# Performance work log

Hardware: AMD Instinct MI355X
Metric: run time of the kernel (lower is better)

Reference implementation:

```python
import jax, jax.numpy as jnp
import numpy as np

N = 100000          # nodes
E = 1600000         # edges (avg degree 16)
IN_DIM = 64
HID = 64
OUT = 32
NUM_GRAPHS = 64


def setup_inputs() -> dict:
    key = jax.random.key(0)
    ks = jax.random.split(key, 12)
    x = jax.random.normal(ks[0], (N, IN_DIM), dtype=jnp.float32)
    edge_index = jax.random.randint(ks[1], (2, E), 0, N, dtype=jnp.int64)
    batch = jnp.sort(jax.random.randint(ks[2], (N,), 0, NUM_GRAPHS, dtype=jnp.int64))
    s = 0.05
    return {
        "x": x,
        "edge_index": edge_index,
        "batch": batch,
        "w1_init": jax.random.normal(ks[3], (IN_DIM, HID), dtype=jnp.float32) * s,
        "w1_root": jax.random.normal(ks[4], (IN_DIM, HID), dtype=jnp.float32) * s,
        "b1": jnp.zeros((HID,), dtype=jnp.float32),
        "w2_init": jax.random.normal(ks[5], (HID, HID), dtype=jnp.float32) * s,
        "w2_root": jax.random.normal(ks[6], (HID, HID), dtype=jnp.float32) * s,
        "b2": jnp.zeros((HID,), dtype=jnp.float32),
        "fc_w": jax.random.normal(ks[7], (HID, OUT), dtype=jnp.float32) * s,
        "fc_b": jnp.zeros((OUT,), dtype=jnp.float32),
    }


def reference(x, edge_index, batch, w1_init, w1_root, b1, w2_init, w2_root, b2, fc_w, fc_b):
    row, col = edge_index[0], edge_index[1]
    # gcn_norm without self loops (ARMAConv default): deg over target nodes
    ones_e = jnp.ones((E,), dtype=x.dtype)
    deg = jax.ops.segment_sum(ones_e, col, num_segments=N)
    dinv = jnp.where(deg > 0, jax.lax.rsqrt(jnp.maximum(deg, 1.0)), 0.0)
    norm = dinv[row] * dinv[col]  # [E]

    def propagate(h):  # out[col] += norm * h[row]
        return jax.ops.segment_sum(h[row] * norm[:, None], col, num_segments=N)

    # ARMAConv (K=1, T=1, act=None): A_hat (x W_init) + x W_root + b
    h = jax.nn.relu(propagate(x @ w1_init) + x @ w1_root + b1)
    h = jax.nn.relu(propagate(h @ w2_init) + h @ w2_root + b2)

    # global mean pool over graphs
    cnt = jax.ops.segment_sum(jnp.ones((N,), dtype=h.dtype), batch, num_segments=NUM_GRAPHS)
    pooled = jax.ops.segment_sum(h, batch, num_segments=NUM_GRAPHS) / jnp.maximum(cnt, 1.0)[:, None]

    return pooled @ fc_w + fc_b  # [NUM_GRAPHS, OUT]
```

## Files before the change

kernel.cpp:

```cpp
#include <hip/hip_runtime.h>
#include <hip/hip_bf16.h>


#define NB 256
#define CAP 5120
#define MAXB 400
#define P1_CHUNK 2048

typedef unsigned int uint32;
typedef unsigned short ushort16;
typedef __attribute__((ext_vector_type(8))) short short8;
typedef __attribute__((ext_vector_type(4))) float f32x4;

__device__ inline uint32 bf16rn(float f) {
    uint32 u = __float_as_uint(f);
    uint32 r = ((u >> 16) & 1u) + 0x7FFFu;
    return (u + r) >> 16;
}
__device__ inline uint32 pack_bf16(float a, float b) {
    return bf16rn(a) | (bf16rn(b) << 16);
}
__device__ inline float bflo(uint32 u) { return __uint_as_float(u << 16); }
__device__ inline float bfhi(uint32 u) { return __uint_as_float(u & 0xFFFF0000u); }

__global__ __launch_bounds__(256) void bucket_kernel(
    const int* __restrict__ row, const int* __restrict__ col,
    uint32* __restrict__ bpack, int* __restrict__ bcnt, int E,
    const float* __restrict__ W1i, const float* __restrict__ W1r,
    const float* __restrict__ W2i, const float* __restrict__ W2r,
    ushort16* __restrict__ wt) {
    __shared__ int hist[MAXB];
    __shared__ int ofs[MAXB];
    __shared__ int cur[MAXB];
    __shared__ int gbase[MAXB];
    __shared__ int s[256];
    __shared__ uint32 stage[P1_CHUNK];
    __shared__ unsigned short stage_bk[P1_CHUNK];

    int t = threadIdx.x;

    if (blockIdx.x < 128) {
        int idx = blockIdx.x * 256 + t;
        int m = idx >> 12;
        int r = idx & 4095;
        int d = r >> 6, k = r & 63;
        const float* W = (m < 2) ? W1i : (m < 4) ? W1r : (m < 6) ? W2i : W2r;
        float v = W[k * 64 + d];
        uint32 hi = bf16rn(v);
        uint32 outv;
        if (m & 1) {
            float hf = __uint_as_float(hi << 16);
            outv = bf16rn(v - hf);
        } else {
            outv = hi;
        }
        wt[(size_t)m * 4096 + d * 64 + k] = (unsigned short)outv;
        return;
    }

    for (int i = t; i < MAXB; i += 256) hist[i] = 0;
    __syncthreads();

    int e0 = (blockIdx.x - 128) * P1_CHUNK;
    int cntE = min(E - e0, P1_CHUNK);

    for (int i = t; i < cntE; i += 256) {
        int c = col[e0 + i];
        atomicAdd(&hist[c >> 8], 1);
    }
    __syncthreads();

    int i2 = 2 * t;
    int a = (i2 < MAXB) ? hist[i2] : 0;
    int b = (i2 + 1 < MAXB) ? hist[i2 + 1] : 0;
    s[t] = a + b;
    __syncthreads();
    for (int off = 1; off < 256; off <<= 1) {
        int x = (t >= off) ? s[t - off] : 0;
        __syncthreads();
        s[t] += x;
        __syncthreads();
    }
    int excl = (t > 0) ? s[t - 1] : 0;
    if (i2 < MAXB) ofs[i2] = excl;
    if (i2 + 1 < MAXB) ofs[i2 + 1] = excl + a;
    __syncthreads();

    for (int i = t; i < MAXB; i += 256) {
        cur[i] = ofs[i];
        gbase[i] = hist[i] ? atomicAdd(&bcnt[i], hist[i]) : 0;
    }
    __syncthreads();

    for (int i = t; i < cntE; i += 256) {
        int c = col[e0 + i];
        int r = row[e0 + i];
        int bk = c >> 8;
        int k = atomicAdd(&cur[bk], 1);
        stage[k] = ((uint32)(c & 255) << 24) | (uint32)r;
        stage_bk[k] = (unsigned short)bk;
    }
    __syncthreads();

    for (int i = t; i < cntE; i += 256) {
        uint32 pk = stage[i];
        int bk = stage_bk[i];
        int gd = gbase[bk] + (i - ofs[bk]);
        if (gd < CAP) bpack[(size_t)bk * CAP + gd] = pk;
    }
}

__global__ __launch_bounds__(1024) void csr_gemm(
    const uint32* __restrict__ bpack, const int* __restrict__ bcnt,
    int* __restrict__ es, int* __restrict__ nstart, int* __restrict__ ndeg,
    float* __restrict__ dinv,
    const float* __restrict__ X, const ushort16* __restrict__ wt4,
    const float* __restrict__ bias,
    ushort16* __restrict__ Ts, ushort16* __restrict__ Rs, int n) {
    __shared__ int h[NB];
    __shared__ alignas(16) unsigned char uni[36864];
    uint32* sbp = (uint32*)uni;
    int* s      = (int*)(uni + 20480);
    int* cur    = (int*)(uni + 21504);
    unsigned short* sXs = (unsigned short*)uni;

    int b = blockIdx.x, t = threadIdx.x;
    if (t < NB) h[t] = 0;
    __syncthreads();
    int cnt = min(bcnt[b], CAP);
    size_t base = (size_t)b * CAP;
    for (int i = t; i < cnt; i += 1024) {
        uint32 pk = bpack[base + i];
        sbp[i] = pk;
        atomicAdd(&h[pk >> 24], 1);
    }
    __syncthreads();
    if (t < NB) s[t] = h[t];
    __syncthreads();
    for (int off = 1; off < NB; off <<= 1) {
        int x = 0;
        if (t < NB && t >= off) x = s[t - off];
        __syncthreads();
        if (t < NB) s[t] += x;
        __syncthreads();
    }
    if (t < NB) {
        int myofs = s[t] - h[t];
        cur[t] = myofs;
        int node = b * NB + t;
        if (node < n) {
            nstart[node] = (int)base + myofs;
            ndeg[node] = h[t];
            dinv[node] = h[t] ? rsqrtf((float)h[t]) : 0.0f;
        }
    }
    __syncthreads();
    for (int i = t; i < cnt; i += 1024) {
        uint32 pk = sbp[i];
        int cl = (int)(pk >> 24);
        int p = atomicAdd(&cur[cl], 1);
        es[base + p] = (int)(pk & 0xFFFFFFu);
    }
    __syncthreads();

    for (int i = t; i < 4096; i += 1024) {
        int tile = i >> 10, j = i & 1023;
        int r = j >> 4, c4 = (j & 15) * 4;
        int node = b * NB + tile * 64 + r;
        float4 v = make_float4(0.f, 0.f, 0.f, 0.f);
        if (node < n) v = *(const float4*)&X[(size_t)node * 64 + c4];
        *(uint32*)&sXs[tile * 4608 + r * 72 + c4] = pack_bf16(v.x, v.y);
        *(uint32*)&sXs[tile * 4608 + r * 72 + c4 + 2] = pack_bf16(v.z, v.w);
    }
    __syncthreads();

    int wv = t >> 6, lane = t & 63;
    int tile = wv >> 2, wq = wv & 3;
    int q = lane >> 4, colx = lane & 15;
    int dim = wq * 16 + colx;

    short8 bih[2], bil[2], brh[2], brl[2];
#pragma unroll
    for (int kh = 0; kh < 2; ++kh) {
        size_t o = (size_t)dim * 64 + kh * 32 + q * 8;
        bih[kh] = *(const short8*)&wt4[0 * 4096 + o];
        bil[kh] = *(const short8*)&wt4[1 * 4096 + o];
        brh[kh] = *(const short8*)&wt4[2 * 4096 + o];
        brl[kh] = *(const short8*)&wt4[3 * 4096 + o];
    }
    float4 bias4 = *(const float4*)&bias[wq * 16 + q * 4];

    unsigned short* TsU = (unsigned short*)Ts;
    unsigned short* RsU = (unsigned short*)Rs;

#pragma unroll
    for (int mt = 0; mt < 4; ++mt) {
        int rbase = mt * 16 + colx;
        short8 a0 = *(const short8*)&sXs[tile * 4608 + rbase * 72 + q * 8];
        short8 a1 = *(const short8*)&sXs[tile * 4608 + rbase * 72 + 32 + q * 8];
        f32x4 accT = {0.f, 0.f, 0.f, 0.f};
        f32x4 accR = {0.f, 0.f, 0.f, 0.f};
        accT = __builtin_amdgcn_mfma_f32_16x16x32_bf16(bih[0], a0, accT, 0, 0, 0);
        accT = __builtin_amdgcn_mfma_f32_16x16x32_bf16(bih[1], a1, accT, 0, 0, 0);
        accT = __builtin_amdgcn_mfma_f32_16x16x32_bf16(bil[0], a0, accT, 0, 0, 0);
        accT = __builtin_amdgcn_mfma_f32_16x16x32_bf16(bil[1], a1, accT, 0, 0, 0);
        accR = __builtin_amdgcn_mfma_f32_16x16x32_bf16(brh[0], a0, accR, 0, 0, 0);
        accR = __builtin_amdgcn_mfma_f32_16x16x32_bf16(brh[1], a1, accR, 0, 0, 0);
        accR = __builtin_amdgcn_mfma_f32_16x16x32_bf16(brl[0], a0, accR, 0, 0, 0);
        accR = __builtin_amdgcn_mfma_f32_16x16x32_bf16(brl[1], a1, accR, 0, 0, 0);

        int li = tile * 64 + mt * 16 + colx;
        int node = b * NB + li;
        if (node < n) {
            int dg = h[li];
            float dv = dg ? rsqrtf((float)dg) : 0.0f;
            uint2 pT, pR;
            pT.x = pack_bf16(accT[0] * dv, accT[1] * dv);
            pT.y = pack_bf16(accT[2] * dv, accT[3] * dv);
            pR.x = pack_bf16(accR[0] + bias4.x, accR[1] + bias4.y);
            pR.y = pack_bf16(accR[2] + bias4.z, accR[3] + bias4.w);
            size_t o = (size_t)node * 64 + wq * 16 + q * 4;
            *(uint2*)&TsU[o] = pT;
            *(uint2*)&RsU[o] = pR;
        }
    }
}

__global__ __launch_bounds__(256) void gather_gemm(
    const uint2* __restrict__ Ts2, const uint2* __restrict__ Rs2,
    const int* __restrict__ es, const int* __restrict__ nstart,
    const int* __restrict__ ndeg, const float* __restrict__ dinv,
    const ushort16* __restrict__ wt4, const float* __restrict__ bias,
    ushort16* __restrict__ To, ushort16* __restrict__ Ro, int n) {
    __shared__ unsigned short sHs[64 * 72];
    int t = threadIdx.x;
    int w = t >> 6, lane = t & 63;
    int q = lane >> 4, d4 = lane & 15;
    int node0 = blockIdx.x * 64;

    for (int rd = 0; rd < 16; ++rd) {
        int cl = w * 16 + rd;
        int c = node0 + cl;
        if (c < n) {
            int deg = ndeg[c];
            int s0 = nstart[c];
            float a0 = 0.f, a1 = 0.f, a2 = 0.f, a3 = 0.f;
            for (int base = 0; base < deg; base += 64) {
                int m = min(deg - base, 64);
                int sid = (lane < m) ? es[s0 + base + lane] : 0;
                for (int j = 0; j < m; j += 16) {
                    int e0 = j + q, e1 = j + 4 + q, e2 = j + 8 + q, e3 = j + 12 + q;
                    int r0 = __shfl(sid, e0);
                    int r1 = __shfl(sid, e1);
                    int r2 = __shfl(sid, e2);
                    int r3 = __shfl(sid, e3);
                    uint2 z = make_uint2(0u, 0u);
                    uint2 v0 = (e0 < m) ? Ts2[(size_t)r0 * 16 + d4] : z;
                    uint2 v1 = (e1 < m) ? Ts2[(size_t)r1 * 16 + d4] : z;
                    uint2 v2 = (e2 < m) ? Ts2[(size_t)r2 * 16 + d4] : z;
                    uint2 v3 = (e3 < m) ? Ts2[(size_t)r3 * 16 + d4] : z;
                    a0 += bflo(v0.x) + bflo(v1.x) + bflo(v2.x) + bflo(v3.x);
                    a1 += bfhi(v0.x) + bfhi(v1.x) + bfhi(v2.x) + bfhi(v3.x);
                    a2 += bflo(v0.y) + bflo(v1.y) + bflo(v2.y) + bflo(v3.y);
                    a3 += bfhi(v0.y) + bfhi(v1.y) + bfhi(v2.y) + bfhi(v3.y);
                }
            }
            a0 += __shfl_xor(a0, 16); a0 += __shfl_xor(a0, 32);
            a1 += __shfl_xor(a1, 16); a1 += __shfl_xor(a1, 32);
            a2 += __shfl_xor(a2, 16); a2 += __shfl_xor(a2, 32);
            a3 += __shfl_xor(a3, 16); a3 += __shfl_xor(a3, 32);
            if (lane < 16) {
                float dc = dinv[c];
                uint2 ur = Rs2[(size_t)c * 16 + d4];
                float h0 = fmaxf(fmaf(dc, a0, bflo(ur.x)), 0.0f);
                float h1 = fmaxf(fmaf(dc, a1, bfhi(ur.x)), 0.0f);
                float h2 = fmaxf(fmaf(dc, a2, bflo(ur.y)), 0.0f);
                float h3 = fmaxf(fmaf(dc, a3, bfhi(ur.y)), 0.0f);
                *(uint2*)&sHs[cl * 72 + d4 * 4] =
                    make_uint2(pack_bf16(h0, h1), pack_bf16(h2, h3));
            }
        } else {
            if (lane < 16)
                *(uint2*)&sHs[cl * 72 + d4 * 4] = make_uint2(0u, 0u);
        }
    }
    __syncthreads();

    int colx = lane & 15;
    int dim = w * 16 + colx;

    short8 bih[2], bil[2], brh[2], brl[2];
#pragma unroll
    for (int kh = 0; kh < 2; ++kh) {
        size_t o = (size_t)dim * 64 + kh * 32 + q * 8;
        bih[kh] = *(const short8*)&wt4[0 * 4096 + o];
        bil[kh] = *(const short8*)&wt4[1 * 4096 + o];
        brh[kh] = *(const short8*)&wt4[2 * 4096 + o];
        brl[kh] = *(const short8*)&wt4[3 * 4096 + o];
    }
    float4 bias4 = *(const float4*)&bias[w * 16 + q * 4];

    unsigned short* ToU = (unsigned short*)To;
    unsigned short* RoU = (unsigned short*)Ro;

#pragma unroll
    for (int mt = 0; mt < 4; ++mt) {
        int rbase = mt * 16 + colx;
        short8 a0 = *(const short8*)&sHs[rbase * 72 + q * 8];
        short8 a1 = *(const short8*)&sHs[rbase * 72 + 32 + q * 8];
        f32x4 accT = {0.f, 0.f, 0.f, 0.f};
        f32x4 accR = {0.f, 0.f, 0.f, 0.f};
        accT = __builtin_amdgcn_mfma_f32_16x16x32_bf16(bih[0], a0, accT, 0, 0, 0);
        accT = __builtin_amdgcn_mfma_f32_16x16x32_bf16(bih[1], a1, accT, 0, 0, 0);
        accT = __builtin_amdgcn_mfma_f32_16x16x32_bf16(bil[0], a0, accT, 0, 0, 0);
        accT = __builtin_amdgcn_mfma_f32_16x16x32_bf16(bil[1], a1, accT, 0, 0, 0);
        accR = __builtin_amdgcn_mfma_f32_16x16x32_bf16(brh[0], a0, accR, 0, 0, 0);
        accR = __builtin_amdgcn_mfma_f32_16x16x32_bf16(brh[1], a1, accR, 0, 0, 0);
        accR = __builtin_amdgcn_mfma_f32_16x16x32_bf16(brl[0], a0, accR, 0, 0, 0);
        accR = __builtin_amdgcn_mfma_f32_16x16x32_bf16(brl[1], a1, accR, 0, 0, 0);

        int node = node0 + mt * 16 + colx;
        if (node < n) {
            float dv = dinv[node];
            uint2 pT, pR;
            pT.x = pack_bf16(accT[0] * dv, accT[1] * dv);
            pT.y = pack_bf16(accT[2] * dv, accT[3] * dv);
            pR.x = pack_bf16(accR[0] + bias4.x, accR[1] + bias4.y);
            pR.y = pack_bf16(accR[2] + bias4.z, accR[3] + bias4.w);
            size_t o = (size_t)node * 64 + w * 16 + q * 4;
            *(uint2*)&ToU[o] = pT;
            *(uint2*)&RoU[o] = pR;
        }
    }
}

__global__ __launch_bounds__(256) void gather_fused(
    const uint2* __restrict__ Ts2, const uint2* __restrict__ Rs2,
    const int* __restrict__ es, const int* __restrict__ nstart,
    const int* __restrict__ ndeg, const float* __restrict__ dinv,
    uint2* __restrict__ Hb2, int n) {
    int c = blockIdx.x * 4 + (threadIdx.x >> 6);
    if (c >= n) return;
    int lane = threadIdx.x & 63;
    int q = lane >> 4;
    int d4 = lane & 15;
    int deg = ndeg[c];
    int s0 = nstart[c];
    float a0 = 0.f, a1 = 0.f, a2 = 0.f, a3 = 0.f;
    for (int base = 0; base < deg; base += 64) {
        int m = min(deg - base, 64);
        int sid = (lane < m) ? es[s0 + base + lane] : 0;
        for (int j = 0; j < m; j += 16) {
            int e0 = j + q, e1 = j + 4 + q, e2 = j + 8 + q, e3 = j + 12 + q;
            int r0 = __shfl(sid, e0);
            int r1 = __shfl(sid, e1);
            int r2 = __shfl(sid, e2);
            int r3 = __shfl(sid, e3);
            uint2 z = make_uint2(0u, 0u);
            uint2 v0 = (e0 < m) ? Ts2[(size_t)r0 * 16 + d4] : z;
            uint2 v1 = (e1 < m) ? Ts2[(size_t)r1 * 16 + d4] : z;
            uint2 v2 = (e2 < m) ? Ts2[(size_t)r2 * 16 + d4] : z;
            uint2 v3 = (e3 < m) ? Ts2[(size_t)r3 * 16 + d4] : z;
            a0 += bflo(v0.x) + bflo(v1.x) + bflo(v2.x) + bflo(v3.x);
            a1 += bfhi(v0.x) + bfhi(v1.x) + bfhi(v2.x) + bfhi(v3.x);
            a2 += bflo(v0.y) + bflo(v1.y) + bflo(v2.y) + bflo(v3.y);
            a3 += bfhi(v0.y) + bfhi(v1.y) + bfhi(v2.y) + bfhi(v3.y);
        }
    }
    a0 += __shfl_xor(a0, 16); a0 += __shfl_xor(a0, 32);
    a1 += __shfl_xor(a1, 16); a1 += __shfl_xor(a1, 32);
    a2 += __shfl_xor(a2, 16); a2 += __shfl_xor(a2, 32);
    a3 += __shfl_xor(a3, 16); a3 += __shfl_xor(a3, 32);
    if (lane < 16) {
        float dc = dinv[c];
        uint2 ur = Rs2[(size_t)c * 16 + d4];
        float h0 = fmaxf(fmaf(dc, a0, bflo(ur.x)), 0.0f);
        float h1 = fmaxf(fmaf(dc, a1, bfhi(ur.x)), 0.0f);
        float h2 = fmaxf(fmaf(dc, a2, bflo(ur.y)), 0.0f);
        float h3 = fmaxf(fmaf(dc, a3, bfhi(ur.y)), 0.0f);
        Hb2[(size_t)c * 16 + d4] = make_uint2(pack_bf16(h0, h1), pack_bf16(h2, h3));
    }
}

__global__ __launch_bounds__(256) void pool_kernel(
    const uint32* __restrict__ Hb, const int* __restrict__ batch,
    float* __restrict__ pooled, float* __restrict__ cnt, int n) {
    __shared__ float sAcc[64 * 64];
    __shared__ float sCnt[64];
    int tid = threadIdx.x;
    for (int i = tid; i < 4096; i += 256) sAcc[i] = 0.0f;
    if (tid < 64) sCnt[tid] = 0.0f;
    __syncthreads();

    int w = tid >> 6, lane = tid & 63;
    int half = lane >> 5, d2 = lane & 31;
    int s = blockIdx.x * 64 + w * 16;
    int e = min(s + 16, n);
    float a0 = 0.0f, a1 = 0.0f, c = 0.0f;
    int gcur = -1;
    for (int i = s + half; i < e; i += 2) {
        int g = batch[i];
        if (g != gcur) {
            if (gcur >= 0) {
                atomicAdd(&sAcc[gcur * 64 + 2 * d2], a0);
                atomicAdd(&sAcc[gcur * 64 + 2 * d2 + 1], a1);
                if (d2 == 0) atomicAdd(&sCnt[gcur], c);
            }
            gcur = g; a0 = 0.0f; a1 = 0.0f; c = 0.0f;
        }
        uint32 u = Hb[(size_t)i * 32 + d2];
        a0 += bflo(u);
        a1 += bfhi(u);
        c += 1.0f;
    }
    if (gcur >= 0) {
        atomicAdd(&sAcc[gcur * 64 + 2 * d2], a0);
        atomicAdd(&sAcc[gcur * 64 + 2 * d2 + 1], a1);
        if (d2 == 0) atomicAdd(&sCnt[gcur], c);
    }
    __syncthreads();
    for (int i = tid; i < 4096; i += 256) {
        float v = sAcc[i];
        if (v != 0.0f) atomicAdd(&pooled[i], v);
    }
    if (tid < 64) {
        float v = sCnt[tid];
        if (v != 0.0f) atomicAdd(&cnt[tid], v);
    }
}

__global__ void final_fc(const float* __restrict__ pooled, const float* __restrict__ cnt,
                         const float* __restrict__ fcw, const float* __restrict__ fcb,
                         float* __restrict__ out) {
    int idx = blockIdx.x * 256 + threadIdx.x;
    if (idx >= 64 * 32) return;
    int g = idx >> 5, o = idx & 31;
    float c = fmaxf(cnt[g], 1.0f);
    float acc = 0.0f;
#pragma unroll
    for (int k = 0; k < 64; ++k) acc = fmaf(pooled[g * 64 + k], fcw[k * 32 + o], acc);
    out[idx] = acc / c + fcb[o];
}

extern "C" void kernel_launch(void* const* d_in, const int* in_sizes, int n_in,
                              void* d_out, int out_size, void* d_ws, size_t ws_size,
                              hipStream_t stream) {
    const float* x       = (const float*)d_in[0];
    const int*   eidx    = (const int*)d_in[1];
    const int*   batch   = (const int*)d_in[2];
    const float* w1_init = (const float*)d_in[3];
    const float* w1_root = (const float*)d_in[4];
    const float* b1      = (const float*)d_in[5];
    const float* w2_init = (const float*)d_in[6];
    const float* w2_root = (const float*)d_in[7];
    const float* b2      = (const float*)d_in[8];
    const float* fc_w    = (const float*)d_in[9];
    const float* fc_b    = (const float*)d_in[10];
    float* out = (float*)d_out;

    const int N = in_sizes[0] / 64;
    const int E = in_sizes[1] / 2;
    const int* row = eidx;
    const int* col = eidx + E;

    const int B = (N + NB - 1) / NB;

    uint32* bpack = (uint32*)d_ws;
    int*   es     = (int*)(bpack + (size_t)B * CAP);
    int*   bcnt   = es + (size_t)B * CAP;
    float* pooled = (float*)(bcnt + MAXB);
    float* cnt    = pooled + 64 * 64;
    int*   nstart = (int*)(cnt + 64);
    int*   ndeg   = nstart + N;
    float* dinv   = (float*)(ndeg + N);
    uint32* wtU   = (uint32*)(dinv + N);
    uint32* Ts1   = wtU + 16384;
    uint32* Rs1   = Ts1 + (size_t)N * 32;
    uint32* T2    = Rs1 + (size_t)N * 32;
    uint32* R2    = T2 + (size_t)N * 32;
    ushort16* wt  = (ushort16*)wtU;

    hipMemsetAsync(bcnt, 0, (size_t)(MAXB + 64 * 64 + 64) * sizeof(int), stream);

    const int EB = (E + P1_CHUNK - 1) / P1_CHUNK;
    bucket_kernel<<<128 + EB, 256, 0, stream>>>(row, col, bpack, bcnt, E,
                                                w1_init, w1_root, w2_init, w2_root, wt);

    csr_gemm<<<B, 1024, 0, stream>>>(bpack, bcnt, es, nstart, ndeg, dinv,
                                     x, wt, b1, (ushort16*)Ts1, (ushort16*)Rs1, N);

    gather_gemm<<<(N + 63) / 64, 256, 0, stream>>>(
        (const uint2*)Ts1, (const uint2*)Rs1, es, nstart, ndeg, dinv,
        wt + (size_t)4 * 4096, b2, (ushort16*)T2, (ushort16*)R2, N);

    gather_fused<<<(N + 3) / 4, 256, 0, stream>>>(
        (const uint2*)T2, (const uint2*)R2, es, nstart, ndeg, dinv,
        (uint2*)Ts1, N);

    pool_kernel<<<(N + 63) / 64, 256, 0, stream>>>(Ts1, batch, pooled, cnt, N);
    final_fc<<<(64 * 32 + 255) / 256, 256, 0, stream>>>(pooled, cnt, fc_w, fc_b, out);
}
```

Measured before the change: 282.0 us.

## Fuse final layer gather with global mean pooling

```diff
diff --git a/kernel.cpp b/kernel.cpp
--- a/kernel.cpp
+++ b/kernel.cpp
@@ -334,98 +334,99 @@
     }
 }
 
-__global__ __launch_bounds__(256) void gather_fused(
+__global__ __launch_bounds__(256) void gather_pool(
     const uint2* __restrict__ Ts2, const uint2* __restrict__ Rs2,
     const int* __restrict__ es, const int* __restrict__ nstart,
     const int* __restrict__ ndeg, const float* __restrict__ dinv,
-    uint2* __restrict__ Hb2, int n) {
-    int c = blockIdx.x * 4 + (threadIdx.x >> 6);
-    if (c >= n) return;
-    int lane = threadIdx.x & 63;
-    int q = lane >> 4;
-    int d4 = lane & 15;
-    int deg = ndeg[c];
-    int s0 = nstart[c];
-    float a0 = 0.f, a1 = 0.f, a2 = 0.f, a3 = 0.f;
-    for (int base = 0; base < deg; base += 64) {
-        int m = min(deg - base, 64);
-        int sid = (lane < m) ? es[s0 + base + lane] : 0;
-        for (int j = 0; j < m; j += 16) {
-            int e0 = j + q, e1 = j + 4 + q, e2 = j + 8 + q, e3 = j + 12 + q;
-            int r0 = __shfl(sid, e0);
-            int r1 = __shfl(sid, e1);
-            int r2 = __shfl(sid, e2);
-            int r3 = __shfl(sid, e3);
-            uint2 z = make_uint2(0u, 0u);
-            uint2 v0 = (e0 < m) ? Ts2[(size_t)r0 * 16 + d4] : z;
-            uint2 v1 = (e1 < m) ? Ts2[(size_t)r1 * 16 + d4] : z;
-            uint2 v2 = (e2 < m) ? Ts2[(size_t)r2 * 16 + d4] : z;
-            uint2 v3 = (e3 < m) ? Ts2[(size_t)r3 * 16 + d4] : z;
-            a0 += bflo(v0.x) + bflo(v1.x) + bflo(v2.x) + bflo(v3.x);
-            a1 += bfhi(v0.x) + bfhi(v1.x) + bfhi(v2.x) + bfhi(v3.x);
-            a2 += bflo(v0.y) + bflo(v1.y) + bflo(v2.y) + bflo(v3.y);
-            a3 += bfhi(v0.y) + bfhi(v1.y) + bfhi(v2.y) + bfhi(v3.y);
-        }
-    }
-    a0 += __shfl_xor(a0, 16); a0 += __shfl_xor(a0, 32);
-    a1 += __shfl_xor(a1, 16); a1 += __shfl_xor(a1, 32);
-    a2 += __shfl_xor(a2, 16); a2 += __shfl_xor(a2, 32);
-    a3 += __shfl_xor(a3, 16); a3 += __shfl_xor(a3, 32);
-    if (lane < 16) {
-        float dc = dinv[c];
-        uint2 ur = Rs2[(size_t)c * 16 + d4];
-        float h0 = fmaxf(fmaf(dc, a0, bflo(ur.x)), 0.0f);
-        float h1 = fmaxf(fmaf(dc, a1, bfhi(ur.x)), 0.0f);
-        float h2 = fmaxf(fmaf(dc, a2, bflo(ur.y)), 0.0f);
-        float h3 = fmaxf(fmaf(dc, a3, bfhi(ur.y)), 0.0f);
-        Hb2[(size_t)c * 16 + d4] = make_uint2(pack_bf16(h0, h1), pack_bf16(h2, h3));
-    }
-}
-
-__global__ __launch_bounds__(256) void pool_kernel(
-    const uint32* __restrict__ Hb, const int* __restrict__ batch,
+    const int* __restrict__ batch,
     float* __restrict__ pooled, float* __restrict__ cnt, int n) {
     __shared__ float sAcc[64 * 64];
     __shared__ float sCnt[64];
-    int tid = threadIdx.x;
-    for (int i = tid; i < 4096; i += 256) sAcc[i] = 0.0f;
-    if (tid < 64) sCnt[tid] = 0.0f;
-    __syncthreads();
-
-    int w = tid >> 6, lane = tid & 63;
-    int half = lane >> 5, d2 = lane & 31;
-    int s = blockIdx.x * 64 + w * 16;
-    int e = min(s + 16, n);
-    float a0 = 0.0f, a1 = 0.0f, c = 0.0f;
+    int t = threadIdx.x;
+    for (int i = t; i < 4096; i += 256) sAcc[i] = 0.0f;
+    if (t < 64) sCnt[t] = 0.0f;
+    __syncthreads();
+
+    int w = t >> 6, lane = t & 63;
+    int q = lane >> 4, d4 = lane & 15;
+    int node0 = blockIdx.x * 64;
+
     int gcur = -1;
-    for (int i = s + half; i < e; i += 2) {
-        int g = batch[i];
-        if (g != gcur) {
-            if (gcur >= 0) {
-                atomicAdd(&sAcc[gcur * 64 + 2 * d2], a0);
-                atomicAdd(&sAcc[gcur * 64 + 2 * d2 + 1], a1);
-                if (d2 == 0) atomicAdd(&sCnt[gcur], c);
+    float p0 = 0.f, p1 = 0.f, p2 = 0.f, p3 = 0.f, pc = 0.f;
+
+    for (int rd = 0; rd < 16; ++rd) {
+        int c = node0 + w * 16 + rd;
+        if (c < n) {
+            int g = batch[c];
+            if (g != gcur) {
+                if (gcur >= 0 && lane < 16) {
+                    atomicAdd(&sAcc[gcur * 64 + d4 * 4 + 0], p0);
+                    atomicAdd(&sAcc[gcur * 64 + d4 * 4 + 1], p1);
+                    atomicAdd(&sAcc[gcur * 64 + d4 * 4 + 2], p2);
+                    atomicAdd(&sAcc[gcur * 64 + d4 * 4 + 3], p3);
+                    if (d4 == 0) atomicAdd(&sCnt[gcur], pc);
+                }
+                gcur = g;
+                p0 = p1 = p2 = p3 = 0.f; pc = 0.f;
             }
-            gcur = g; a0 = 0.0f; a1 = 0.0f; c = 0.0f;
+            int deg = ndeg[c];
+            int s0 = nstart[c];
+            float a0 = 0.f, a1 = 0.f, a2 = 0.f, a3 = 0.f;
+            for (int base = 0; base < deg; base += 64) {
+                int m = min(deg - base, 64);
+                int sid = (lane < m) ? es[s0 + base + lane] : 0;
+                for (int j = 0; j < m; j += 16) {
+                    int e0 = j + q, e1 = j + 4 + q, e2 = j + 8 + q, e3 = j + 12 + q;
+                    int r0 = __shfl(sid, e0);
+                    int r1 = __shfl(sid, e1);
+                    int r2 = __shfl(sid, e2);
+                    int r3 = __shfl(sid, e3);
+                    uint2 z = make_uint2(0u, 0u);
+                    uint2 v0 = (e0 < m) ? Ts2[(size_t)r0 * 16 + d4] : z;
+                    uint2 v1 = (e1 < m) ? Ts2[(size_t)r1 * 16 + d4] : z;
+                    uint2 v2 = (e2 < m) ? Ts2[(size_t)r2 * 16 + d4] : z;
+                    uint2 v3 = (e3 < m) ? Ts2[(size_t)r3 * 16 + d4] : z;
+                    a0 += bflo(v0.x) + bflo(v1.x) + bflo(v2.x) + bflo(v3.x);
+                    a1 += bfhi(v0.x) + bfhi(v1.x) + bfhi(v2.x) + bfhi(v3.x);
+                    a2 += bflo(v0.y) + bflo(v1.y) + bflo(v2.y) + bflo(v3.y);
+                    a3 += bfhi(v0.y) + bfhi(v1.y) + bfhi(v2.y) + bfhi(v3.y);
+                }
+            }
+            a0 += __shfl_xor(a0, 16); a0 += __shfl_xor(a0, 32);
+            a1 += __shfl_xor(a1, 16); a1 += __shfl_xor(a1, 32);
+            a2 += __shfl_xor(a2, 16); a2 += __shfl_xor(a2, 32);
+            a3 += __shfl_xor(a3, 16); a3 += __shfl_xor(a3, 32);
+            if (lane < 16) {
+                float dc = dinv[c];
+                uint2 ur = Rs2[(size_t)c * 16 + d4];
+                float h0 = fmaxf(fmaf(dc, a0, bflo(ur.x)), 0.0f);
+                float h1 = fmaxf(fmaf(dc, a1, bfhi(ur.x)), 0.0f);
+                float h2 = fmaxf(fmaf(dc, a2, bflo(ur.y)), 0.0f);
+                float h3 = fmaxf(fmaf(dc, a3, bfhi(ur.y)), 0.0f);
+                uint2 hb = make_uint2(pack_bf16(h0, h1), pack_bf16(h2, h3));
+                p0 += bflo(hb.x);
+                p1 += bfhi(hb.x);
+                p2 += bflo(hb.y);
+                p3 += bfhi(hb.y);
+                if (d4 == 0) pc += 1.0f;
+            }
         }
-        uint32 u = Hb[(size_t)i * 32 + d2];
-        a0 += bflo(u);
-        a1 += bfhi(u);
-        c += 1.0f;
-    }
-    if (gcur >= 0) {
-        atomicAdd(&sAcc[gcur * 64 + 2 * d2], a0);
-        atomicAdd(&sAcc[gcur * 64 + 2 * d2 + 1], a1);
-        if (d2 == 0) atomicAdd(&sCnt[gcur], c);
-    }
-    __syncthreads();
-    for (int i = tid; i < 4096; i += 256) {
+    }
+    if (gcur >= 0 && lane < 16) {
+        atomicAdd(&sAcc[gcur * 64 + d4 * 4 + 0], p0);
+        atomicAdd(&sAcc[gcur * 64 + d4 * 4 + 1], p1);
+        atomicAdd(&sAcc[gcur * 64 + d4 * 4 + 2], p2);
+        atomicAdd(&sAcc[gcur * 64 + d4 * 4 + 3], p3);
+        if (d4 == 0) atomicAdd(&sCnt[gcur], pc);
+    }
+    __syncthreads();
+    for (int i = t; i < 4096; i += 256) {
         float v = sAcc[i];
         if (v != 0.0f) atomicAdd(&pooled[i], v);
     }
-    if (tid < 64) {
-        float v = sCnt[tid];
-        if (v != 0.0f) atomicAdd(&cnt[tid], v);
+    if (t < 64) {
+        float v = sCnt[t];
+        if (v != 0.0f) atomicAdd(&cnt[t], v);
     }
 }
 
@@ -493,10 +494,9 @@
         (const uint2*)Ts1, (const uint2*)Rs1, es, nstart, ndeg, dinv,
         wt + (size_t)4 * 4096, b2, (ushort16*)T2, (ushort16*)R2, N);
 
-    gather_fused<<<(N + 3) / 4, 256, 0, stream>>>(
+    gather_pool<<<(N + 63) / 64, 256, 0, stream>>>(
         (const uint2*)T2, (const uint2*)R2, es, nstart, ndeg, dinv,
-        (uint2*)Ts1, N);
-
-    pool_kernel<<<(N + 63) / 64, 256, 0, stream>>>(Ts1, batch, pooled, cnt, N);
+        batch, pooled, cnt, N);
+
     final_fc<<<(64 * 32 + 255) / 256, 256, 0, stream>>>(pooled, cnt, fc_w, fc_b, out);
 }
```

After: 272.3 us, median of 2. 3.4% less time.
